# Performance work log

Measured on AMD Instinct MI355X. Metric: run time of the kernel, lower is better.

The kernel has to match this reference:

```python
import jax, jax.numpy as jnp
import numpy as np

B, N, E = 8, 2000, 32000
LAT, STY, NF = 128, 64, 10
HEADS, HID = 4, 128
OUT = 3 + NF  # 13
EPS = 1e-5
SLOPE = 0.2


def _lin(k, fi, fo):
    return jax.random.normal(k, (fi, fo), dtype=jnp.float32) / np.sqrt(fi)


def setup_inputs() -> dict:
    key = jax.random.key(0)
    ks = jax.random.split(key, 32)
    inp = {
        'z': jax.random.normal(ks[0], (B, LAT), dtype=jnp.float32),
        'template_x': jax.random.normal(ks[1], (N, NF), dtype=jnp.float32),
        'template_edge_index': jax.random.randint(ks[2], (2, E), 0, N, dtype=jnp.int32),
        # style MLP
        'mlp_w1': _lin(ks[3], LAT, 256), 'mlp_b1': jnp.zeros((256,), jnp.float32),
        'mlp_w2': _lin(ks[4], 256, 512), 'mlp_b2': jnp.zeros((512,), jnp.float32),
        'mlp_w3': _lin(ks[5], 512, STY), 'mlp_b3': jnp.zeros((STY,), jnp.float32),
        # GAT1: in = NF + STY = 74 -> heads*HID = 512, concat
        'gat1_w': _lin(ks[6], NF + STY, HEADS * HID),
        'gat1_as': jax.random.normal(ks[7], (HEADS, HID), jnp.float32) * 0.1,
        'gat1_ad': jax.random.normal(ks[8], (HEADS, HID), jnp.float32) * 0.1,
        'gat1_b': jnp.zeros((HEADS * HID,), jnp.float32),
        'ln1_g': jnp.ones((HEADS * HID,), jnp.float32), 'ln1_b': jnp.zeros((HEADS * HID,), jnp.float32),
        # GAT2: 512 -> 512, concat
        'gat2_w': _lin(ks[9], HEADS * HID, HEADS * HID),
        'gat2_as': jax.random.normal(ks[10], (HEADS, HID), jnp.float32) * 0.1,
        'gat2_ad': jax.random.normal(ks[11], (HEADS, HID), jnp.float32) * 0.1,
        'gat2_b': jnp.zeros((HEADS * HID,), jnp.float32),
        'ln2_g': jnp.ones((HEADS * HID,), jnp.float32), 'ln2_b': jnp.zeros((HEADS * HID,), jnp.float32),
        # GAT3: 512 -> 13, 1 head, no concat
        'gat3_w': _lin(ks[12], HEADS * HID, OUT),
        'gat3_as': jax.random.normal(ks[13], (1, OUT), jnp.float32) * 0.1,
        'gat3_ad': jax.random.normal(ks[14], (1, OUT), jnp.float32) * 0.1,
        'gat3_b': jnp.zeros((OUT,), jnp.float32),
    }
    return inp


def gat_conv(x, src, dst, n_nodes, W, a_src, a_dst, bias, heads, out_ch, concat):
    # x: [NT, F_in]; per-head linear transform
    h = (x @ W).reshape(-1, heads, out_ch)              # [NT, H, C]
    als = jnp.sum(h * a_src[None], axis=-1)             # [NT, H]
    ald = jnp.sum(h * a_dst[None], axis=-1)             # [NT, H]
    logits = jax.nn.leaky_relu(als[src] + ald[dst], SLOPE)   # [E, H]
    # segment softmax over destination nodes (self-loops guarantee nonempty segments)
    mx = jax.ops.segment_max(logits, dst, num_segments=n_nodes)
    alpha = jnp.exp(logits - mx[dst])
    den = jax.ops.segment_sum(alpha, dst, num_segments=n_nodes)
    alpha = alpha / den[dst]                             # [E, H]
    msgs = h[src] * alpha[:, :, None]                    # [E, H, C]
    out = jax.ops.segment_sum(msgs, dst, num_segments=n_nodes)  # [NT, H, C]
    if concat:
        return out.reshape(n_nodes, heads * out_ch) + bias
    return out.mean(axis=1) + bias


def layer_norm(x, g, b):
    mu = jnp.mean(x, axis=-1, keepdims=True)
    var = jnp.mean((x - mu) ** 2, axis=-1, keepdims=True)
    return (x - mu) * jax.lax.rsqrt(var + EPS) * g + b


def reference(z, template_x, template_edge_index,
              mlp_w1, mlp_b1, mlp_w2, mlp_b2, mlp_w3, mlp_b3,
              gat1_w, gat1_as, gat1_ad, gat1_b, ln1_g, ln1_b,
              gat2_w, gat2_as, gat2_ad, gat2_b, ln2_g, ln2_b,
              gat3_w, gat3_as, gat3_ad, gat3_b):
    bsz = z.shape[0]
    n = template_x.shape[0]
    nt = bsz * n
    # batch the template graph: replicate nodes, offset edge indices per graph
    x = jnp.tile(template_x, (bsz, 1))                                  # [NT, NF]
    off = (jnp.arange(bsz, dtype=template_edge_index.dtype) * n)
    ei = (template_edge_index[:, None, :] + off[None, :, None]).reshape(2, -1)  # [2, B*E]
    loops = jnp.arange(nt, dtype=ei.dtype)
    src = jnp.concatenate([ei[0], loops])
    dst = jnp.concatenate([ei[1], loops])
    # style MLP
    s = jax.nn.leaky_relu(z @ mlp_w1 + mlp_b1, SLOPE)
    s = jax.nn.leaky_relu(s @ mlp_w2 + mlp_b2, SLOPE)
    s = s @ mlp_w3 + mlp_b3                                             # [B, STY]
    s_exp = jnp.repeat(s, n, axis=0)                                    # [NT, STY]
    H0 = jnp.concatenate([x, s_exp], axis=1)
    H1 = jax.nn.leaky_relu(gat_conv(H0, src, dst, nt, gat1_w, gat1_as, gat1_ad, gat1_b, HEADS, HID, True), SLOPE)
    H1n = layer_norm(H1, ln1_g, ln1_b)
    H2 = jax.nn.leaky_relu(gat_conv(H1n, src, dst, nt, gat2_w, gat2_as, gat2_ad, gat2_b, HEADS, HID, True), SLOPE)
    H2 = H2 + H1n
    H2n = layer_norm(H2, ln2_g, ln2_b)
    H_out = gat_conv(H2n, src, dst, nt, gat3_w, gat3_as, gat3_ad, gat3_b, 1, OUT, False)  # [NT, 13]
    delta_p = H_out[:, :3]
    delta_f = H_out[:, 3:]
    p_gen = x[:, :3] + delta_p
    X_gen = jnp.concatenate([p_gen, x[:, 3:] + delta_f[:, 3:]], axis=1)  # X[:, :3] overwritten by p_gen
    EF = p_gen[ei[1]] - p_gen[ei[0]]                                     # edge displacement vectors [B*E, 3]
    return X_gen, p_gen, EF
```

## Files before the change

kernel.cpp:

```cpp
#include <hip/hip_runtime.h>
#include <hip/hip_fp16.h>

constexpr int Bz = 8, Nn = 2000, Ee = 32000, NTOT = 16000;
constexpr int XG_OFF = 0, PG_OFF = 160000, EF_OFF = 208000;
#define SLOPE 0.2f
#define EPSL 1e-5f

typedef __attribute__((ext_vector_type(8))) _Float16 f16x8;
typedef __attribute__((ext_vector_type(4))) float float4v;

__device__ __forceinline__ float lrelu(float x) { return x > 0.f ? x : SLOPE * x; }

__device__ __forceinline__ unsigned short f2h(float x) {
  _Float16 hh = (_Float16)x;
  return *(unsigned short*)&hh;
}

__device__ __forceinline__ float wave_max(float v) {
  for (int o = 32; o; o >>= 1) v = fmaxf(v, __shfl_xor(v, o));
  return v;
}
__device__ __forceinline__ float wave_sum(float v) {
  for (int o = 32; o; o >>= 1) v += __shfl_xor(v, o);
  return v;
}

__global__ void hist_k(const int* __restrict__ tei, int* __restrict__ counts) {
  int j = blockIdx.x * 256 + threadIdx.x;
  if (j < Ee) atomicAdd(&counts[tei[Ee + j]], 1);
}

__global__ void scan_k(const int* __restrict__ counts, int* __restrict__ offs) {
  __shared__ int part[256];
  int t = threadIdx.x;
  int loc[8];
  int s = 0;
  for (int i = 0; i < 8; i++) {
    int idx = t * 8 + i;
    int c = (idx < Nn) ? counts[idx] : 0;
    loc[i] = s; s += c;
  }
  part[t] = s;
  __syncthreads();
  for (int o = 1; o < 256; o <<= 1) {
    int v = (t >= o) ? part[t - o] : 0;
    __syncthreads();
    part[t] += v;
    __syncthreads();
  }
  int excl = (t == 0) ? 0 : part[t - 1];
  for (int i = 0; i < 8; i++) {
    int idx = t * 8 + i;
    if (idx < Nn) offs[idx] = excl + loc[i];
  }
  if (t == 255) offs[Nn] = part[255];
}

__global__ void place_k(const int* __restrict__ tei, const int* __restrict__ offs,
                        int* __restrict__ cursor, int* __restrict__ colb) {
  int j = blockIdx.x * 256 + threadIdx.x;
  if (j < Ee) {
    int d = tei[Ee + j];
    int slot = offs[d] + atomicAdd(&cursor[d], 1);
    colb[slot] = tei[j];
  }
}

template <int K, int ACT>
__global__ __launch_bounds__(256) void lin_k(const float* __restrict__ x, const float* __restrict__ w,
                                             const float* __restrict__ bias, float* __restrict__ y,
                                             int O) {
  int gw = blockIdx.x * 4 + (threadIdx.x >> 6);
  int lane = threadIdx.x & 63;
  int bb = gw / O, o = gw - bb * O;
  float acc = 0.f;
#pragma unroll
  for (int k = lane; k < K; k += 64) acc += x[bb * K + k] * w[k * O + o];
  acc = wave_sum(acc);
  if (lane == 0) {
    if (bias) acc += bias[o];
    y[gw] = ACT ? lrelu(acc) : acc;
  }
}

__global__ __launch_bounds__(256) void w2bf_k(const float* __restrict__ W, unsigned short* __restrict__ Bt) {
  __shared__ float tile[32][33];
  int tx = threadIdx.x & 31, ty = threadIdx.x >> 5;
  int x0 = blockIdx.x * 32;
  int y0 = blockIdx.y * 32;
  for (int r = ty; r < 32; r += 8) tile[r][tx] = W[(y0 + r) * 512 + x0 + tx];
  __syncthreads();
  for (int r = ty; r < 32; r += 8) {
    unsigned short v = f2h(tile[tx][r]);
    size_t off = (size_t)(x0 + r) * 512 + (y0 + tx);
#pragma unroll
    for (int cp = 0; cp < 8; cp++) Bt[cp * 262144 + off] = v;
  }
}

__global__ void w3t_k(const float* __restrict__ W, unsigned short* __restrict__ W3t) {
  for (int idx = threadIdx.x; idx < 8192; idx += 256) {
    int col = idx >> 9, k = idx & 511;
    float v = (col < 13) ? W[k * 13 + col] : 0.f;
    W3t[idx] = f2h(v);
  }
}

__global__ __launch_bounds__(256) void tp16_k(const float* __restrict__ tx, const float* __restrict__ g1w,
                                              const float* __restrict__ a_s, const float* __restrict__ a_d,
                                              unsigned short* __restrict__ tp16, float* __restrict__ tpa,
                                              float* __restrict__ tpd) {
  int nl = blockIdx.x;
  int head = threadIdx.x >> 6, lane = threadIdx.x & 63;
  int c = head * 128 + 2 * lane;
  float t0 = 0.f, t1 = 0.f;
#pragma unroll
  for (int k = 0; k < 10; k++) {
    float xv = tx[nl * 10 + k];
    float2 wv = *(const float2*)&g1w[k * 512 + c];
    t0 += xv * wv.x; t1 += xv * wv.y;
  }
  ushort2 st; st.x = f2h(t0); st.y = f2h(t1);
  *(ushort2*)&tp16[(size_t)nl * 512 + c] = st;
  float2 av = *(const float2*)&a_s[c];
  float2 dv = *(const float2*)&a_d[c];
  float pa = wave_sum(t0 * av.x + t1 * av.y);
  float pd = wave_sum(t0 * dv.x + t1 * dv.y);
  if (lane == 0) { tpa[nl * 4 + head] = pa; tpd[nl * 4 + head] = pd; }
}

__global__ void pba_k(const float* __restrict__ pb, const float* __restrict__ a_s,
                      const float* __restrict__ a_d, float* __restrict__ pba, float* __restrict__ pbd) {
  int b = blockIdx.x >> 2, h = blockIdx.x & 3;
  int lane = threadIdx.x;
  int c = h * 128 + 2 * lane;
  float2 pv = *(const float2*)&pb[b * 512 + c];
  float2 av = *(const float2*)&a_s[c];
  float2 dv = *(const float2*)&a_d[c];
  float pa = wave_sum(pv.x * av.x + pv.y * av.y);
  float pd = wave_sum(pv.x * dv.x + pv.y * dv.y);
  if (lane == 0) { pba[b * 4 + h] = pa; pbd[b * 4 + h] = pd; }
}

__global__ __launch_bounds__(256) void agg1_k(const unsigned short* __restrict__ tp16,
                                              const float* __restrict__ tpa, const float* __restrict__ tpd,
                                              const float* __restrict__ pba, const float* __restrict__ pbd,
                                              const float* __restrict__ pb,
                                              const float* __restrict__ bias,
                                              const float* __restrict__ g, const float* __restrict__ beta,
                                              unsigned short* __restrict__ out,
                                              const int* __restrict__ offs, const int* __restrict__ colb) {
  int blk = blockIdx.x;
  int b = blk & 7, nl = blk >> 3;
  int n = b * Nn + nl;
  int w = threadIdx.x >> 6, lane = threadIdx.x & 63;
  int rs = offs[nl];
  int nit = offs[nl + 1] - rs + 1;
  float aldn = tpd[nl * 4 + w] + pbd[b * 4 + w];
  float pbsrc = pba[b * 4 + w];

  __shared__ unsigned int alpha_u[4][68];
  __shared__ int sgn[64];
  __shared__ float part[4][512];
  __shared__ float invs[4];
  __shared__ float red[8];
  __shared__ float bcs[2];

  __half2 acc2[4];
#pragma unroll
  for (int j = 0; j < 4; j++) acc2[j] = __float2half2_rn(0.f);

  const unsigned short* hbase = tp16 + lane * 8;
  int hd = lane >> 4;

  if (nit <= 64) {
    int se = nl;
    float logit = -3e38f;
    if (lane < nit) {
      se = (lane < nit - 1) ? colb[rs + lane] : nl;
      logit = lrelu(tpa[se * 4 + w] + pbsrc + aldn);
    }
    if (w == 0) sgn[lane] = se;
    float m = wave_max(logit);
    float raw = (lane < nit) ? __expf(logit - m) : 0.f;
    float den = wave_sum(raw);
    if (lane == 0) invs[w] = 1.f / den;
    __half2 a2 = __float2half2_rn(raw);
    alpha_u[w][lane] = *(unsigned int*)&a2;
    __syncthreads();
    int e = w;
    for (; e + 12 < nit; e += 16) {
      uint4 hv[4];
      unsigned int au[4];
#pragma unroll
      for (int i = 0; i < 4; i++) {
        int ei = e + i * 4;
        au[i] = alpha_u[hd][ei];
        hv[i] = *(const uint4*)(hbase + (size_t)sgn[ei] * 512);
      }
#pragma unroll
      for (int i = 0; i < 4; i++) {
        __half2 a2e = *(__half2*)&au[i];
        acc2[0] = __hfma2(a2e, *(__half2*)&hv[i].x, acc2[0]);
        acc2[1] = __hfma2(a2e, *(__half2*)&hv[i].y, acc2[1]);
        acc2[2] = __hfma2(a2e, *(__half2*)&hv[i].z, acc2[2]);
        acc2[3] = __hfma2(a2e, *(__half2*)&hv[i].w, acc2[3]);
      }
    }
    for (; e < nit; e += 4) {
      unsigned int au = alpha_u[hd][e];
      uint4 hv = *(const uint4*)(hbase + (size_t)sgn[e] * 512);
      __half2 a2e = *(__half2*)&au;
      acc2[0] = __hfma2(a2e, *(__half2*)&hv.x, acc2[0]);
      acc2[1] = __hfma2(a2e, *(__half2*)&hv.y, acc2[1]);
      acc2[2] = __hfma2(a2e, *(__half2*)&hv.z, acc2[2]);
      acc2[3] = __hfma2(a2e, *(__half2*)&hv.w, acc2[3]);
    }
  } else {
    float m = -3e38f;
    for (int i = lane; i < nit; i += 64) {
      int se = (i < nit - 1) ? colb[rs + i] : nl;
      m = fmaxf(m, lrelu(tpa[se * 4 + w] + pbsrc + aldn));
    }
    m = wave_max(m);
    float den = 0.f;
    for (int base = 0; base < nit; base += 64) {
      int cnt = min(64, nit - base);
      int se = nl;
      float raw = 0.f;
      if (lane < cnt) {
        int i = base + lane;
        se = (i < nit - 1) ? colb[rs + i] : nl;
        raw = __expf(lrelu(tpa[se * 4 + w] + pbsrc + aldn) - m);
      }
      if (w == 0) sgn[lane] = se;
      den += raw;
      __half2 a2 = __float2half2_rn(raw);
      alpha_u[w][lane] = *(unsigned int*)&a2;
      __syncthreads();
      for (int e = w; e < cnt; e += 4) {
        unsigned int au = alpha_u[hd][e];
        uint4 hv = *(const uint4*)(hbase + (size_t)sgn[e] * 512);
        __half2 a2e = *(__half2*)&au;
        acc2[0] = __hfma2(a2e, *(__half2*)&hv.x, acc2[0]);
        acc2[1] = __hfma2(a2e, *(__half2*)&hv.y, acc2[1]);
        acc2[2] = __hfma2(a2e, *(__half2*)&hv.z, acc2[2]);
        acc2[3] = __hfma2(a2e, *(__half2*)&hv.w, acc2[3]);
      }
      __syncthreads();
    }
    den = wave_sum(den);
    if (lane == 0) invs[w] = 1.f / den;
  }

  float fv[8];
#pragma unroll
  for (int j = 0; j < 4; j++) {
    float2 f2 = __half22float2(acc2[j]);
    fv[2 * j] = f2.x; fv[2 * j + 1] = f2.y;
  }
  *(float4*)&part[w][lane * 8] = make_float4(fv[0], fv[1], fv[2], fv[3]);
  *(float4*)&part[w][lane * 8 + 4] = make_float4(fv[4], fv[5], fv[6], fv[7]);
  __syncthreads();

  int c = 2 * (int)threadIdx.x;
  float inv = invs[c >> 7];
  float s0 = part[0][c] + part[1][c] + part[2][c] + part[3][c];
  float s1 = part[0][c + 1] + part[1][c + 1] + part[2][c + 1] + part[3][c + 1];
  float2 pv = *(const float2*)&pb[b * 512 + c];
  float v0 = lrelu(s0 * inv + pv.x + bias[c]);
  float v1 = lrelu(s1 * inv + pv.y + bias[c + 1]);
  float p1 = wave_sum(v0 + v1);
  float p2 = wave_sum(v0 * v0 + v1 * v1);
  if (lane == 0) { red[w] = p1; red[4 + w] = p2; }
  __syncthreads();
  if (threadIdx.x == 0) {
    float s1r = red[0] + red[1] + red[2] + red[3];
    float s2r = red[4] + red[5] + red[6] + red[7];
    float mu = s1r * (1.f / 512.f);
    float var = s2r * (1.f / 512.f) - mu * mu;
    bcs[0] = mu;
    bcs[1] = rsqrtf(var + EPSL);
  }
  __syncthreads();
  float mu = bcs[0], rstd = bcs[1];
  float o0 = (v0 - mu) * rstd * g[c] + beta[c];
  float o1 = (v1 - mu) * rstd * g[c + 1] + beta[c + 1];
  ushort2 st; st.x = f2h(o0); st.y = f2h(o1);
  *(ushort2*)&out[(size_t)n * 512 + c] = st;
}

__global__ __launch_bounds__(256) void agg_k(const unsigned short* __restrict__ h,
                                             const float* __restrict__ als, const float* __restrict__ ald,
                                             const float* __restrict__ bias,
                                             const float* __restrict__ g, const float* __restrict__ beta,
                                             const unsigned short* __restrict__ resid,
                                             unsigned short* __restrict__ out,
                                             const int* __restrict__ offs, const int* __restrict__ colb) {
  int blk = blockIdx.x;
  int b = blk & 7, nl = blk >> 3;
  int n = b * Nn + nl;
  int w = threadIdx.x >> 6, lane = threadIdx.x & 63;
  int rs = offs[nl];
  int nit = offs[nl + 1] - rs + 1;
  float aldn = ald[n * 4 + w];

  __shared__ unsigned int alpha_u[4][68];
  __shared__ int sgn[64];
  __shared__ float part[4][512];
  __shared__ float invs[4];
  __shared__ float red[8];
  __shared__ float bcs[2];

  __half2 acc2[4];
#pragma unroll
  for (int j = 0; j < 4; j++) acc2[j] = __float2half2_rn(0.f);

  const unsigned short* hbase = h + lane * 8;
  int hd = lane >> 4;

  if (nit <= 64) {
    int sg = n;
    float logit = -3e38f;
    if (lane < nit) {
      sg = (lane < nit - 1) ? colb[rs + lane] + b * Nn : n;
      logit = lrelu(als[sg * 4 + w] + aldn);
    }
    if (w == 0) sgn[lane] = sg;
    float m = wave_max(logit);
    float raw = (lane < nit) ? __expf(logit - m) : 0.f;
    float den = wave_sum(raw);
    if (lane == 0) invs[w] = 1.f / den;
    __half2 a2 = __float2half2_rn(raw);
    alpha_u[w][lane] = *(unsigned int*)&a2;
    __syncthreads();
    int e = w;
    for (; e + 12 < nit; e += 16) {
      uint4 hv[4];
      unsigned int au[4];
#pragma unroll
      for (int i = 0; i < 4; i++) {
        int ei = e + i * 4;
        au[i] = alpha_u[hd][ei];
        hv[i] = *(const uint4*)(hbase + (size_t)sgn[ei] * 512);
      }
#pragma unroll
      for (int i = 0; i < 4; i++) {
        __half2 a2e = *(__half2*)&au[i];
        acc2[0] = __hfma2(a2e, *(__half2*)&hv[i].x, acc2[0]);
        acc2[1] = __hfma2(a2e, *(__half2*)&hv[i].y, acc2[1]);
        acc2[2] = __hfma2(a2e, *(__half2*)&hv[i].z, acc2[2]);
        acc2[3] = __hfma2(a2e, *(__half2*)&hv[i].w, acc2[3]);
      }
    }
    for (; e < nit; e += 4) {
      unsigned int au = alpha_u[hd][e];
      uint4 hv = *(const uint4*)(hbase + (size_t)sgn[e] * 512);
      __half2 a2e = *(__half2*)&au;
      acc2[0] = __hfma2(a2e, *(__half2*)&hv.x, acc2[0]);
      acc2[1] = __hfma2(a2e, *(__half2*)&hv.y, acc2[1]);
      acc2[2] = __hfma2(a2e, *(__half2*)&hv.z, acc2[2]);
      acc2[3] = __hfma2(a2e, *(__half2*)&hv.w, acc2[3]);
    }
  } else {
    float m = -3e38f;
    for (int i = lane; i < nit; i += 64) {
      int sg = (i < nit - 1) ? colb[rs + i] + b * Nn : n;
      m = fmaxf(m, lrelu(als[sg * 4 + w] + aldn));
    }
    m = wave_max(m);
    float den = 0.f;
    for (int base = 0; base < nit; base += 64) {
      int cnt = min(64, nit - base);
      int sg = n;
      float raw = 0.f;
      if (lane < cnt) {
        int i = base + lane;
        sg = (i < nit - 1) ? colb[rs + i] + b * Nn : n;
        raw = __expf(lrelu(als[sg * 4 + w] + aldn) - m);
      }
      if (w == 0) sgn[lane] = sg;
      den += raw;
      __half2 a2 = __float2half2_rn(raw);
      alpha_u[w][lane] = *(unsigned int*)&a2;
      __syncthreads();
      for (int e = w; e < cnt; e += 4) {
        unsigned int au = alpha_u[hd][e];
        uint4 hv = *(const uint4*)(hbase + (size_t)sgn[e] * 512);
        __half2 a2e = *(__half2*)&au;
        acc2[0] = __hfma2(a2e, *(__half2*)&hv.x, acc2[0]);
        acc2[1] = __hfma2(a2e, *(__half2*)&hv.y, acc2[1]);
        acc2[2] = __hfma2(a2e, *(__half2*)&hv.z, acc2[2]);
        acc2[3] = __hfma2(a2e, *(__half2*)&hv.w, acc2[3]);
      }
      __syncthreads();
    }
    den = wave_sum(den);
    if (lane == 0) invs[w] = 1.f / den;
  }

  float fv[8];
#pragma unroll
  for (int j = 0; j < 4; j++) {
    float2 f2 = __half22float2(acc2[j]);
    fv[2 * j] = f2.x; fv[2 * j + 1] = f2.y;
  }
  *(float4*)&part[w][lane * 8] = make_float4(fv[0], fv[1], fv[2], fv[3]);
  *(float4*)&part[w][lane * 8 + 4] = make_float4(fv[4], fv[5], fv[6], fv[7]);
  __syncthreads();

  int c = 2 * (int)threadIdx.x;
  float inv = invs[c >> 7];
  float s0 = part[0][c] + part[1][c] + part[2][c] + part[3][c];
  float s1 = part[0][c + 1] + part[1][c + 1] + part[2][c + 1] + part[3][c + 1];
  float v0 = lrelu(s0 * inv + bias[c]);
  float v1 = lrelu(s1 * inv + bias[c + 1]);
  unsigned int rv = *(const unsigned int*)&resid[(size_t)n * 512 + c];
  __half2 rh = *(__half2*)&rv;
  float2 rf = __half22float2(rh);
  v0 += rf.x; v1 += rf.y;
  float p1 = wave_sum(v0 + v1);
  float p2 = wave_sum(v0 * v0 + v1 * v1);
  if (lane == 0) { red[w] = p1; red[4 + w] = p2; }
  __syncthreads();
  if (threadIdx.x == 0) {
    float s1r = red[0] + red[1] + red[2] + red[3];
    float s2r = red[4] + red[5] + red[6] + red[7];
    float mu = s1r * (1.f / 512.f);
    float var = s2r * (1.f / 512.f) - mu * mu;
    bcs[0] = mu;
    bcs[1] = rsqrtf(var + EPSL);
  }
  __syncthreads();
  float mu = bcs[0], rstd = bcs[1];
  float o0 = (v0 - mu) * rstd * g[c] + beta[c];
  float o1 = (v1 - mu) * rstd * g[c + 1] + beta[c + 1];
  ushort2 st; st.x = f2h(o0); st.y = f2h(o1);
  *(ushort2*)&out[(size_t)n * 512 + c] = st;
}

__global__ __launch_bounds__(256) void gemm2_k(const unsigned short* __restrict__ A,
                                               const unsigned short* __restrict__ Bt,
                                               unsigned short* __restrict__ C,
                                               const float* __restrict__ As, const float* __restrict__ Ad,
                                               float* __restrict__ als2, float* __restrict__ ald2) {
  __shared__ unsigned short sB[64][520];
  int t = threadIdx.x;
  int lane = t & 63, w = t >> 6;
  int m0 = blockIdx.x * 128;
  int n0 = blockIdx.y * 64;
  const unsigned short* Bl = Bt + (size_t)((blockIdx.x + blockIdx.y * 125) & 7) * 262144;

#pragma unroll
  for (int q = 0; q < 16; q++) {
    int slot = q * 256 + t;
    int row = slot >> 6, c16 = (slot & 63) * 8;
    *(uint4*)&sB[row][c16] = *(const uint4*)(Bl + (size_t)(n0 + row) * 512 + c16);
  }
  __syncthreads();

  float4v acc[2][4];
#pragma unroll
  for (int m = 0; m < 2; m++)
#pragma unroll
    for (int nn = 0; nn < 4; nn++) acc[m][nn] = (float4v){0.f, 0.f, 0.f, 0.f};

  int r0 = m0 + w * 32 + (lane & 15);
  int kb = (lane >> 4) * 8;
  const unsigned short* a0p = A + (size_t)r0 * 512 + kb;
  const unsigned short* a1p = A + (size_t)(r0 + 16) * 512 + kb;
  int bc = lane & 15;

#pragma unroll
  for (int kf = 0; kf < 16; kf++) {
    int k0 = kf * 32;
    f16x8 af0 = *(const f16x8*)(a0p + k0);
    f16x8 af1 = *(const f16x8*)(a1p + k0);
    f16x8 bg0 = *(const f16x8*)&sB[bc][k0 + kb];
    f16x8 bg1 = *(const f16x8*)&sB[16 + bc][k0 + kb];
    f16x8 bg2 = *(const f16x8*)&sB[32 + bc][k0 + kb];
    f16x8 bg3 = *(const f16x8*)&sB[48 + bc][k0 + kb];
    acc[0][0] = __builtin_amdgcn_mfma_f32_16x16x32_f16(af0, bg0, acc[0][0], 0, 0, 0);
    acc[0][1] = __builtin_amdgcn_mfma_f32_16x16x32_f16(af0, bg1, acc[0][1], 0, 0, 0);
    acc[0][2] = __builtin_amdgcn_mfma_f32_16x16x32_f16(af0, bg2, acc[0][2], 0, 0, 0);
    acc[0][3] = __builtin_amdgcn_mfma_f32_16x16x32_f16(af0, bg3, acc[0][3], 0, 0, 0);
    acc[1][0] = __builtin_amdgcn_mfma_f32_16x16x32_f16(af1, bg0, acc[1][0], 0, 0, 0);
    acc[1][1] = __builtin_amdgcn_mfma_f32_16x16x32_f16(af1, bg1, acc[1][1], 0, 0, 0);
    acc[1][2] = __builtin_amdgcn_mfma_f32_16x16x32_f16(af1, bg2, acc[1][2], 0, 0, 0);
    acc[1][3] = __builtin_amdgcn_mfma_f32_16x16x32_f16(af1, bg3, acc[1][3], 0, 0, 0);
  }

  {
    int head = n0 >> 7;
    int cb = n0 & 127;
    float asv[4], adv[4];
#pragma unroll
    for (int nn = 0; nn < 4; nn++) {
      asv[nn] = As[head * 128 + cb + nn * 16 + bc];
      adv[nn] = Ad[head * 128 + cb + nn * 16 + bc];
    }
#pragma unroll
    for (int m = 0; m < 2; m++) {
#pragma unroll
      for (int r = 0; r < 4; r++) {
        float pa = 0.f, pd = 0.f;
#pragma unroll
        for (int nn = 0; nn < 4; nn++) { pa += acc[m][nn][r] * asv[nn]; pd += acc[m][nn][r] * adv[nn]; }
        for (int o = 1; o < 16; o <<= 1) { pa += __shfl_xor(pa, o); pd += __shfl_xor(pd, o); }
        if ((lane & 15) == 0) {
          int row = m0 + w * 32 + (lane >> 4) * 4 + m * 16 + r;
          atomicAdd(&als2[row * 4 + head], pa);
          atomicAdd(&ald2[row * 4 + head], pd);
        }
      }
    }
  }

  __syncthreads();
  unsigned short* sC = &sB[0][0];
  int rb = w * 32 + (lane >> 4) * 4;
#pragma unroll
  for (int m = 0; m < 2; m++)
#pragma unroll
    for (int nn = 0; nn < 4; nn++)
#pragma unroll
      for (int r = 0; r < 4; r++)
        sC[(rb + m * 16 + r) * 72 + bc + nn * 16] = f2h(acc[m][nn][r]);
  __syncthreads();
#pragma unroll
  for (int p = 0; p < 4; p++) {
    int row = p * 32 + (t >> 3);
    int co = (t & 7) * 8;
    uint4 v = *(const uint4*)&sC[row * 72 + co];
    *(uint4*)&C[(size_t)(m0 + row) * 512 + n0 + co] = v;
  }
}

__global__ __launch_bounds__(256) void gemm3_k(const unsigned short* __restrict__ H,
                                               const unsigned short* __restrict__ W3t,
                                               const float* __restrict__ as3, const float* __restrict__ ad3,
                                               float* __restrict__ h3, float* __restrict__ als3,
                                               float* __restrict__ ald3) {
  int w = threadIdx.x >> 6, l = threadIdx.x & 63;
  int blk = blockIdx.x;
  int b = blk & 7, i = blk >> 3;
  int base = i * 64 + w * 16;
  int r16 = l & 15, g4 = l >> 4;
  int lrow_ld = min(base + r16, Nn - 1);
  float4v acc = (float4v){0.f, 0.f, 0.f, 0.f};
  const unsigned short* ha = H + (size_t)(b * Nn + lrow_ld) * 512 + g4 * 8;
  const unsigned short* wb = W3t + (size_t)r16 * 512 + g4 * 8;
#pragma unroll
  for (int kk = 0; kk < 16; kk++) {
    f16x8 a = *(const f16x8*)(ha + kk * 32);
    f16x8 bfr = *(const f16x8*)(wb + kk * 32);
    acc = __builtin_amdgcn_mfma_f32_16x16x32_f16(a, bfr, acc, 0, 0, 0);
  }
  int col = r16;
  float asv = (col < 13) ? as3[col] : 0.f;
  float adv = (col < 13) ? ad3[col] : 0.f;
#pragma unroll
  for (int r = 0; r < 4; r++) {
    float v = acc[r];
    int lrow = base + g4 * 4 + r;
    if (lrow < Nn) {
      int row = b * Nn + lrow;
      if (col < 13) h3[row * 13 + col] = v;
      float sa = v * asv, sd = v * adv;
      for (int o = 1; o < 16; o <<= 1) { sa += __shfl_xor(sa, o); sd += __shfl_xor(sd, o); }
      if (col == 0) { als3[row] = sa; ald3[row] = sd; }
    }
  }
}

__global__ __launch_bounds__(64) void agg3_k(const float* __restrict__ h3, const float* __restrict__ als3,
                                             const float* __restrict__ ald3, const float* __restrict__ b3,
                                             const float* __restrict__ tx, const int* __restrict__ offs,
                                             const int* __restrict__ colb, float* __restrict__ dout) {
  int blk = blockIdx.x, lane = threadIdx.x;
  int b = blk & 7, nl = blk >> 3;
  int n = b * Nn + nl;
  int rs = offs[nl], deg = offs[nl + 1] - rs;
  float aldn = ald3[n];
  float sl = lrelu(als3[n] + aldn);
  float a = 0.f, inv;
  if (deg <= 64) {
    int sgl = 0; float logit = -1e30f;
    if (lane < deg) { sgl = colb[rs + lane] + b * Nn; logit = lrelu(als3[sgl] + aldn); }
    float m = wave_max(fmaxf(logit, sl));
    float raw = (lane < deg) ? __expf(logit - m) : 0.f;
    float es = __expf(sl - m);
    inv = 1.f / (wave_sum(raw) + es);
    if (lane < 13) a = es * h3[n * 13 + lane];
    for (int e = 0; e < deg; e++) {
      float w = __shfl(raw, e);
      int sg = __shfl(sgl, e);
      if (lane < 13) a += w * h3[sg * 13 + lane];
    }
  } else {
    float m = sl;
    for (int e = lane; e < deg; e += 64) {
      int sg = colb[rs + e] + b * Nn;
      m = fmaxf(m, lrelu(als3[sg] + aldn));
    }
    m = wave_max(m);
    float es = __expf(sl - m);
    float den = (lane == 0) ? es : 0.f;
    if (lane < 13) a = es * h3[n * 13 + lane];
    for (int base = 0; base < deg; base += 64) {
      int cnt = min(64, deg - base);
      int sgl = 0; float raw = 0.f;
      if (lane < cnt) {
        sgl = colb[rs + base + lane] + b * Nn;
        raw = __expf(lrelu(als3[sgl] + aldn) - m);
      }
      den += raw;
      for (int e = 0; e < cnt; e++) {
        float w = __shfl(raw, e);
        int sg = __shfl(sgl, e);
        if (lane < 13) a += w * h3[sg * 13 + lane];
      }
    }
    inv = 1.f / wave_sum(den);
  }
  a *= inv;
  float hv = a + ((lane < 13) ? b3[lane] : 0.f);
  float txv = (lane < 10) ? tx[nl * 10 + lane] : 0.f;
  float pv = txv + hv;
  if (lane < 3) dout[PG_OFF + n * 3 + lane] = pv;
  float up = __shfl(hv, lane + 3);
  float xg = (lane < 3) ? pv : (txv + up);
  if (lane < 10) dout[XG_OFF + n * 10 + lane] = xg;
}

__global__ void ef_k(const int* __restrict__ tei, float* __restrict__ dout) {
  int blk = blockIdx.x;
  int b = blk & 7, i = blk >> 3;
  int j = i * 256 + threadIdx.x;
  int e = b * Ee + j;
  int sg = tei[j] + b * Nn;
  int dg = tei[Ee + j] + b * Nn;
  const float* pg = dout + PG_OFF;
  dout[EF_OFF + e * 3 + 0] = pg[dg * 3 + 0] - pg[sg * 3 + 0];
  dout[EF_OFF + e * 3 + 1] = pg[dg * 3 + 1] - pg[sg * 3 + 1];
  dout[EF_OFF + e * 3 + 2] = pg[dg * 3 + 2] - pg[sg * 3 + 2];
}

extern "C" void kernel_launch(void* const* d_in, const int* in_sizes, int n_in,
                              void* d_out, int out_size, void* d_ws, size_t ws_size,
                              hipStream_t stream) {
  const float* z = (const float*)d_in[0];
  const float* tx = (const float*)d_in[1];
  const int* tei = (const int*)d_in[2];
  const float* w1 = (const float*)d_in[3];
  const float* b1 = (const float*)d_in[4];
  const float* w2 = (const float*)d_in[5];
  const float* b2 = (const float*)d_in[6];
  const float* w3 = (const float*)d_in[7];
  const float* b3 = (const float*)d_in[8];
  const float* g1w = (const float*)d_in[9];
  const float* g1as = (const float*)d_in[10];
  const float* g1ad = (const float*)d_in[11];
  const float* g1b = (const float*)d_in[12];
  const float* ln1g = (const float*)d_in[13];
  const float* ln1b = (const float*)d_in[14];
  const float* g2w = (const float*)d_in[15];
  const float* g2as = (const float*)d_in[16];
  const float* g2ad = (const float*)d_in[17];
  const float* g2b = (const float*)d_in[18];
  const float* ln2g = (const float*)d_in[19];
  const float* ln2b = (const float*)d_in[20];
  const float* g3w = (const float*)d_in[21];
  const float* g3as = (const float*)d_in[22];
  const float* g3ad = (const float*)d_in[23];
  const float* g3b = (const float*)d_in[24];
  float* out = (float*)d_out;

  float* F = (float*)d_ws;
  float* pb_ = F + 0;
  float* l1_ = F + 8192;
  float* l2_ = F + 16384;
  float* s_ = F + 24576;
  float* pba_ = F + 30000;
  float* pbd_ = F + 30100;
  float* tpa_ = F + 100000;
  float* tpd_ = F + 164000;
  float* als2 = F + 228000;
  float* ald2 = F + 292000;
  float* als3 = F + 356000;
  float* ald3 = F + 372000;
  float* h3_ = F + 388000;
  unsigned short* U = (unsigned short*)(F + 600000);
  unsigned short* hA = U;
  unsigned short* hB = U + 8192000;
  unsigned short* Bt = U + 16384000;
  unsigned short* W3t = U + 18481152;
  unsigned short* tp16 = U + 18489344;
  int* I = (int*)(F + 12000000);
  int* counts = I;
  int* cursor = I + 2000;
  int* offs = I + 4000;
  int* colb = I + 6001;

  hipMemsetAsync(counts, 0, 4000 * sizeof(int), stream);
  hipMemsetAsync(als2, 0, 64000 * sizeof(float), stream);
  hipMemsetAsync(ald2, 0, 64000 * sizeof(float), stream);

  hist_k<<<125, 256, 0, stream>>>(tei, counts);
  scan_k<<<1, 256, 0, stream>>>(counts, offs);
  place_k<<<125, 256, 0, stream>>>(tei, offs, cursor, colb);

  w2bf_k<<<dim3(16, 16), 256, 0, stream>>>(g2w, Bt);
  w3t_k<<<1, 256, 0, stream>>>(g3w, W3t);
  tp16_k<<<Nn, 256, 0, stream>>>(tx, g1w, g1as, g1ad, tp16, tpa_, tpd_);

  lin_k<128, 1><<<512, 256, 0, stream>>>(z, w1, b1, l1_, 256);
  lin_k<256, 1><<<1024, 256, 0, stream>>>(l1_, w2, b2, l2_, 512);
  lin_k<512, 0><<<128, 256, 0, stream>>>(l2_, w3, b3, s_, 64);
  lin_k<64, 0><<<1024, 256, 0, stream>>>(s_, g1w + 10 * 512, nullptr, pb_, 512);
  pba_k<<<32, 64, 0, stream>>>(pb_, g1as, g1ad, pba_, pbd_);

  agg1_k<<<NTOT, 256, 0, stream>>>(tp16, tpa_, tpd_, pba_, pbd_, pb_, g1b, ln1g, ln1b,
                                   hB, offs, colb);

  gemm2_k<<<dim3(125, 8), 256, 0, stream>>>(hB, Bt, hA, g2as, g2ad, als2, ald2);
  agg_k<<<NTOT, 256, 0, stream>>>(hA, als2, ald2, g2b, ln2g, ln2b, hB, hB, offs, colb);

  gemm3_k<<<256, 256, 0, stream>>>(hB, W3t, g3as, g3ad, h3_, als3, ald3);
  agg3_k<<<NTOT, 64, 0, stream>>>(h3_, als3, ald3, g3b, tx, offs, colb, out);
  ef_k<<<1000, 256, 0, stream>>>(tei, out);
}
```

Measured before the change: 193.7 us.

## Process all 8 batches per template node in GAT1 aggregation to reuse gathers

The layer-1 aggregation kernel now launches one block per template node instead of one per (batch, node). Each block gathers the shared template features once and accumulates attention-weighted sums for all 8 batch elements in registers, with per-batch softmax max, denominators and LayerNorm computed in a loop. This removes the 8x redundant gather of neighbor rows, at the cost of far fewer blocks (2000), much higher register pressure (32 half2 accumulators plus per-batch state), and a serialized per-batch epilogue with extra barriers.

```diff
diff --git a/kernel.cpp b/kernel.cpp
--- a/kernel.cpp
+++ b/kernel.cpp
@@ -150,144 +150,143 @@
                                               const float* __restrict__ g, const float* __restrict__ beta,
                                               unsigned short* __restrict__ out,
                                               const int* __restrict__ offs, const int* __restrict__ colb) {
-  int blk = blockIdx.x;
-  int b = blk & 7, nl = blk >> 3;
-  int n = b * Nn + nl;
+  int nl = blockIdx.x;
   int w = threadIdx.x >> 6, lane = threadIdx.x & 63;
   int rs = offs[nl];
   int nit = offs[nl + 1] - rs + 1;
-  float aldn = tpd[nl * 4 + w] + pbd[b * 4 + w];
-  float pbsrc = pba[b * 4 + w];
-
-  __shared__ unsigned int alpha_u[4][68];
+  float tpdn = tpd[nl * 4 + w];
+  float cst[8];
+#pragma unroll
+  for (int b = 0; b < 8; b++) cst[b] = pba[b * 4 + w] + tpdn + pbd[b * 4 + w];
+
+  __shared__ unsigned int alpha_u[4][8][64];
   __shared__ int sgn[64];
   __shared__ float part[4][512];
-  __shared__ float invs[4];
+  __shared__ float invs[4][8];
   __shared__ float red[8];
   __shared__ float bcs[2];
 
-  __half2 acc2[4];
-#pragma unroll
-  for (int j = 0; j < 4; j++) acc2[j] = __float2half2_rn(0.f);
+  __half2 acc2[8][4];
+#pragma unroll
+  for (int b = 0; b < 8; b++)
+#pragma unroll
+    for (int j = 0; j < 4; j++) acc2[b][j] = __float2half2_rn(0.f);
+  float den[8];
+  float mreg[8];
+#pragma unroll
+  for (int b = 0; b < 8; b++) { den[b] = 0.f; mreg[b] = -3e38f; }
+
+  for (int base = 0; base < nit; base += 64) {
+    int i = base + lane;
+    float ta = -3e38f;
+    if (i < nit) {
+      int se = (i < nit - 1) ? colb[rs + i] : nl;
+      ta = tpa[se * 4 + w];
+    }
+#pragma unroll
+    for (int b = 0; b < 8; b++) mreg[b] = fmaxf(mreg[b], lrelu(ta + cst[b]));
+  }
+#pragma unroll
+  for (int b = 0; b < 8; b++) mreg[b] = wave_max(mreg[b]);
 
   const unsigned short* hbase = tp16 + lane * 8;
   int hd = lane >> 4;
-
-  if (nit <= 64) {
+  for (int base = 0; base < nit; base += 64) {
+    int i = base + lane;
+    bool valid = i < nit;
     int se = nl;
-    float logit = -3e38f;
-    if (lane < nit) {
-      se = (lane < nit - 1) ? colb[rs + lane] : nl;
-      logit = lrelu(tpa[se * 4 + w] + pbsrc + aldn);
-    }
+    if (valid) se = (i < nit - 1) ? colb[rs + i] : nl;
     if (w == 0) sgn[lane] = se;
-    float m = wave_max(logit);
-    float raw = (lane < nit) ? __expf(logit - m) : 0.f;
-    float den = wave_sum(raw);
-    if (lane == 0) invs[w] = 1.f / den;
-    __half2 a2 = __float2half2_rn(raw);
-    alpha_u[w][lane] = *(unsigned int*)&a2;
-    __syncthreads();
+    float ta = valid ? tpa[se * 4 + w] : 0.f;
+#pragma unroll
+    for (int b = 0; b < 8; b++) {
+      float raw = valid ? __expf(lrelu(ta + cst[b]) - mreg[b]) : 0.f;
+      den[b] += raw;
+      __half2 a2 = __float2half2_rn(raw);
+      alpha_u[w][b][lane] = *(unsigned int*)&a2;
+    }
+    __syncthreads();
+    int cnt = min(64, nit - base);
     int e = w;
-    for (; e + 12 < nit; e += 16) {
-      uint4 hv[4];
-      unsigned int au[4];
-#pragma unroll
-      for (int i = 0; i < 4; i++) {
-        int ei = e + i * 4;
-        au[i] = alpha_u[hd][ei];
-        hv[i] = *(const uint4*)(hbase + (size_t)sgn[ei] * 512);
-      }
-#pragma unroll
-      for (int i = 0; i < 4; i++) {
-        __half2 a2e = *(__half2*)&au[i];
-        acc2[0] = __hfma2(a2e, *(__half2*)&hv[i].x, acc2[0]);
-        acc2[1] = __hfma2(a2e, *(__half2*)&hv[i].y, acc2[1]);
-        acc2[2] = __hfma2(a2e, *(__half2*)&hv[i].z, acc2[2]);
-        acc2[3] = __hfma2(a2e, *(__half2*)&hv[i].w, acc2[3]);
-      }
-    }
-    for (; e < nit; e += 4) {
-      unsigned int au = alpha_u[hd][e];
-      uint4 hv = *(const uint4*)(hbase + (size_t)sgn[e] * 512);
-      __half2 a2e = *(__half2*)&au;
-      acc2[0] = __hfma2(a2e, *(__half2*)&hv.x, acc2[0]);
-      acc2[1] = __hfma2(a2e, *(__half2*)&hv.y, acc2[1]);
-      acc2[2] = __hfma2(a2e, *(__half2*)&hv.z, acc2[2]);
-      acc2[3] = __hfma2(a2e, *(__half2*)&hv.w, acc2[3]);
-    }
-  } else {
-    float m = -3e38f;
-    for (int i = lane; i < nit; i += 64) {
-      int se = (i < nit - 1) ? colb[rs + i] : nl;
-      m = fmaxf(m, lrelu(tpa[se * 4 + w] + pbsrc + aldn));
-    }
-    m = wave_max(m);
-    float den = 0.f;
-    for (int base = 0; base < nit; base += 64) {
-      int cnt = min(64, nit - base);
-      int se = nl;
-      float raw = 0.f;
-      if (lane < cnt) {
-        int i = base + lane;
-        se = (i < nit - 1) ? colb[rs + i] : nl;
-        raw = __expf(lrelu(tpa[se * 4 + w] + pbsrc + aldn) - m);
-      }
-      if (w == 0) sgn[lane] = se;
-      den += raw;
-      __half2 a2 = __float2half2_rn(raw);
-      alpha_u[w][lane] = *(unsigned int*)&a2;
-      __syncthreads();
-      for (int e = w; e < cnt; e += 4) {
-        unsigned int au = alpha_u[hd][e];
-        uint4 hv = *(const uint4*)(hbase + (size_t)sgn[e] * 512);
-        __half2 a2e = *(__half2*)&au;
-        acc2[0] = __hfma2(a2e, *(__half2*)&hv.x, acc2[0]);
-        acc2[1] = __hfma2(a2e, *(__half2*)&hv.y, acc2[1]);
-        acc2[2] = __hfma2(a2e, *(__half2*)&hv.z, acc2[2]);
-        acc2[3] = __hfma2(a2e, *(__half2*)&hv.w, acc2[3]);
-      }
-      __syncthreads();
-    }
-    den = wave_sum(den);
-    if (lane == 0) invs[w] = 1.f / den;
-  }
-
-  float fv[8];
-#pragma unroll
-  for (int j = 0; j < 4; j++) {
-    float2 f2 = __half22float2(acc2[j]);
-    fv[2 * j] = f2.x; fv[2 * j + 1] = f2.y;
-  }
-  *(float4*)&part[w][lane * 8] = make_float4(fv[0], fv[1], fv[2], fv[3]);
-  *(float4*)&part[w][lane * 8 + 4] = make_float4(fv[4], fv[5], fv[6], fv[7]);
-  __syncthreads();
-
-  int c = 2 * (int)threadIdx.x;
-  float inv = invs[c >> 7];
-  float s0 = part[0][c] + part[1][c] + part[2][c] + part[3][c];
-  float s1 = part[0][c + 1] + part[1][c + 1] + part[2][c + 1] + part[3][c + 1];
-  float2 pv = *(const float2*)&pb[b * 512 + c];
-  float v0 = lrelu(s0 * inv + pv.x + bias[c]);
-  float v1 = lrelu(s1 * inv + pv.y + bias[c + 1]);
-  float p1 = wave_sum(v0 + v1);
-  float p2 = wave_sum(v0 * v0 + v1 * v1);
-  if (lane == 0) { red[w] = p1; red[4 + w] = p2; }
-  __syncthreads();
-  if (threadIdx.x == 0) {
-    float s1r = red[0] + red[1] + red[2] + red[3];
-    float s2r = red[4] + red[5] + red[6] + red[7];
-    float mu = s1r * (1.f / 512.f);
-    float var = s2r * (1.f / 512.f) - mu * mu;
-    bcs[0] = mu;
-    bcs[1] = rsqrtf(var + EPSL);
-  }
-  __syncthreads();
-  float mu = bcs[0], rstd = bcs[1];
-  float o0 = (v0 - mu) * rstd * g[c] + beta[c];
-  float o1 = (v1 - mu) * rstd * g[c + 1] + beta[c + 1];
-  ushort2 st; st.x = f2h(o0); st.y = f2h(o1);
-  *(ushort2*)&out[(size_t)n * 512 + c] = st;
+    for (; e + 4 < cnt; e += 8) {
+      uint4 hv0 = *(const uint4*)(hbase + (size_t)sgn[e] * 512);
+      uint4 hv1 = *(const uint4*)(hbase + (size_t)sgn[e + 4] * 512);
+#pragma unroll
+      for (int b = 0; b < 8; b++) {
+        unsigned int au0 = alpha_u[hd][b][e];
+        unsigned int au1 = alpha_u[hd][b][e + 4];
+        __half2 a0 = *(__half2*)&au0;
+        __half2 a1 = *(__half2*)&au1;
+        acc2[b][0] = __hfma2(a0, *(__half2*)&hv0.x, acc2[b][0]);
+        acc2[b][1] = __hfma2(a0, *(__half2*)&hv0.y, acc2[b][1]);
+        acc2[b][2] = __hfma2(a0, *(__half2*)&hv0.z, acc2[b][2]);
+        acc2[b][3] = __hfma2(a0, *(__half2*)&hv0.w, acc2[b][3]);
+        acc2[b][0] = __hfma2(a1, *(__half2*)&hv1.x, acc2[b][0]);
+        acc2[b][1] = __hfma2(a1, *(__half2*)&hv1.y, acc2[b][1]);
+        acc2[b][2] = __hfma2(a1, *(__half2*)&hv1.z, acc2[b][2]);
+        acc2[b][3] = __hfma2(a1, *(__half2*)&hv1.w, acc2[b][3]);
+      }
+    }
+    if (e < cnt) {
+      uint4 hv0 = *(const uint4*)(hbase + (size_t)sgn[e] * 512);
+#pragma unroll
+      for (int b = 0; b < 8; b++) {
+        unsigned int au0 = alpha_u[hd][b][e];
+        __half2 a0 = *(__half2*)&au0;
+        acc2[b][0] = __hfma2(a0, *(__half2*)&hv0.x, acc2[b][0]);
+        acc2[b][1] = __hfma2(a0, *(__half2*)&hv0.y, acc2[b][1]);
+        acc2[b][2] = __hfma2(a0, *(__half2*)&hv0.z, acc2[b][2]);
+        acc2[b][3] = __hfma2(a0, *(__half2*)&hv0.w, acc2[b][3]);
+      }
+    }
+    __syncthreads();
+  }
+#pragma unroll
+  for (int b = 0; b < 8; b++) {
+    float d = wave_sum(den[b]);
+    if (lane == 0) invs[w][b] = 1.f / d;
+  }
+  __syncthreads();
+
+#pragma unroll
+  for (int b = 0; b < 8; b++) {
+    float fv[8];
+#pragma unroll
+    for (int j = 0; j < 4; j++) {
+      float2 f2 = __half22float2(acc2[b][j]);
+      fv[2 * j] = f2.x; fv[2 * j + 1] = f2.y;
+    }
+    *(float4*)&part[w][lane * 8] = make_float4(fv[0], fv[1], fv[2], fv[3]);
+    *(float4*)&part[w][lane * 8 + 4] = make_float4(fv[4], fv[5], fv[6], fv[7]);
+    __syncthreads();
+
+    int c = 2 * (int)threadIdx.x;
+    float inv = invs[c >> 7][b];
+    float s0 = part[0][c] + part[1][c] + part[2][c] + part[3][c];
+    float s1 = part[0][c + 1] + part[1][c + 1] + part[2][c + 1] + part[3][c + 1];
+    float2 pv = *(const float2*)&pb[b * 512 + c];
+    float v0 = lrelu(s0 * inv + pv.x + bias[c]);
+    float v1 = lrelu(s1 * inv + pv.y + bias[c + 1]);
+    float p1 = wave_sum(v0 + v1);
+    float p2 = wave_sum(v0 * v0 + v1 * v1);
+    if (lane == 0) { red[w] = p1; red[4 + w] = p2; }
+    __syncthreads();
+    if (threadIdx.x == 0) {
+      float s1r = red[0] + red[1] + red[2] + red[3];
+      float s2r = red[4] + red[5] + red[6] + red[7];
+      float mu = s1r * (1.f / 512.f);
+      float var = s2r * (1.f / 512.f) - mu * mu;
+      bcs[0] = mu;
+      bcs[1] = rsqrtf(var + EPSL);
+    }
+    __syncthreads();
+    float mu = bcs[0], rstd = bcs[1];
+    float o0 = (v0 - mu) * rstd * g[c] + beta[c];
+    float o1 = (v1 - mu) * rstd * g[c + 1] + beta[c + 1];
+    ushort2 st; st.x = f2h(o0); st.y = f2h(o1);
+    *(ushort2*)&out[(size_t)(b * Nn + nl) * 512 + c] = st;
+    __syncthreads();
+  }
 }
 
 __global__ __launch_bounds__(256) void agg_k(const unsigned short* __restrict__ h,
@@ -720,8 +719,8 @@
   lin_k<64, 0><<<1024, 256, 0, stream>>>(s_, g1w + 10 * 512, nullptr, pb_, 512);
   pba_k<<<32, 64, 0, stream>>>(pb_, g1as, g1ad, pba_, pbd_);
 
-  agg1_k<<<NTOT, 256, 0, stream>>>(tp16, tpa_, tpd_, pba_, pbd_, pb_, g1b, ln1g, ln1b,
-                                   hB, offs, colb);
+  agg1_k<<<Nn, 256, 0, stream>>>(tp16, tpa_, tpd_, pba_, pbd_, pb_, g1b, ln1g, ln1b,
+                                 hB, offs, colb);
 
   gemm2_k<<<dim3(125, 8), 256, 0, stream>>>(hB, Bt, hA, g2as, g2ad, als2, ald2);
   agg_k<<<NTOT, 256, 0, stream>>>(hA, als2, ald2, g2b, ln2g, ln2b, hB, hB, offs, colb);
```

Result: no change. 195.4 us (+0.9%).
